# Optimization experiments

Hardware: AMD Instinct MI355X
Metric: run time of the kernel (lower is better)

Reference implementation:

```python
import jax, jax.numpy as jnp
import numpy as np


def setup_inputs() -> dict:
    key = jax.random.key(0)
    ks = jax.random.split(key, 6)
    B, Q, K = 4, 512, 1024
    Dq, Dk, Dv, H = 512, 512, 512, 128
    return {
        "queries": jax.random.normal(ks[0], (B, Q, Dq), dtype=jnp.float32),
        "keys": jax.random.normal(ks[1], (B, K, Dk), dtype=jnp.float32),
        "values": jax.random.normal(ks[2], (B, K, Dv), dtype=jnp.float32),
        "W_q": jax.random.normal(ks[3], (Dq, H), dtype=jnp.float32) / np.sqrt(Dq),
        "W_k": jax.random.normal(ks[4], (Dk, H), dtype=jnp.float32) / np.sqrt(Dk),
        "w_v": jax.random.normal(ks[5], (H,), dtype=jnp.float32) / np.sqrt(H),
    }


def reference(queries, keys, values, W_q, W_k, w_v):
    # Additive (Bahdanau) attention.
    q = jnp.einsum("bqd,dh->bqh", queries, W_q)          # [B,Q,H]
    k = jnp.einsum("bkd,dh->bkh", keys, W_k)             # [B,K,H]
    features = jnp.tanh(q[:, :, None, :] + k[:, None, :, :])  # [B,Q,K,H]
    scores = jnp.einsum("bqkh,h->bqk", features, w_v)    # [B,Q,K]
    attn = jax.nn.softmax(scores, axis=-1)               # [B,Q,K]
    return jnp.einsum("bqk,bkv->bqv", attn, values)      # [B,Q,Dv]
```

## Files before the change

kernel.cpp:

```cpp
#include <hip/hip_runtime.h>

#define BB   4
#define QS   512
#define KSZ  1024
#define DD   512
#define HH   128
#define DVV  512

typedef unsigned int uint;
typedef unsigned short ushort;
typedef __attribute__((ext_vector_type(8)))  short short8;
typedef __attribute__((ext_vector_type(16))) float f32x16;

__device__ __forceinline__ float rcp_fast(float x)  { return __builtin_amdgcn_rcpf(x); }
__device__ __forceinline__ float exp2_fast(float x) { return __builtin_amdgcn_exp2f(x); }

__device__ __forceinline__ void split1(float v, ushort& h, ushort& l) {
    uint u = __float_as_uint(v);
    h = (ushort)(u >> 16);
    float r = v - __uint_as_float(u & 0xffff0000u);
    l = (ushort)(__float_as_uint(r) >> 16);
}

#define NVT (BB * (KSZ / 32) * (DVV / 32))
#define NQ8 (BB * QS / 8)
#define NK8 (BB * KSZ / 8)

__global__ __launch_bounds__(256) void prep_kernel(
    const float* __restrict__ q,  const float* __restrict__ k,
    const float* __restrict__ val,
    const float* __restrict__ Wq, const float* __restrict__ Wk,
    float* __restrict__ eq, float* __restrict__ ek,
    ushort* __restrict__ vhi, ushort* __restrict__ vlo)
{
    const int id  = blockIdx.x;
    const int tid = threadIdx.x;

    if (id < NVT) {
        __shared__ float Ts[32][33];
        const int b   = id >> 9;
        const int rem = id & 511;
        const int k0  = (rem >> 4) * 32;
        const int n0  = (rem & 15) * 32;
        {
            const int kk = tid >> 3, n4 = (tid & 7) * 4;
            float4 v = *(const float4*)&val[((size_t)b * KSZ + k0 + kk) * DVV + n0 + n4];
            Ts[kk][n4 + 0] = v.x; Ts[kk][n4 + 1] = v.y;
            Ts[kk][n4 + 2] = v.z; Ts[kk][n4 + 3] = v.w;
        }
        __syncthreads();
        {
            const int nn = tid >> 3, k4 = (tid & 7) * 4;
            ushort h[4], l[4];
            #pragma unroll
            for (int i = 0; i < 4; i++) split1(Ts[k4 + i][nn], h[i], l[i]);
            size_t o = ((size_t)b * DVV + n0 + nn) * KSZ + k0 + k4;
            *(ushort4*)&vhi[o] = make_ushort4(h[0], h[1], h[2], h[3]);
            *(ushort4*)&vlo[o] = make_ushort4(l[0], l[1], l[2], l[3]);
        }
        return;
    }

    __shared__ float At[8][36];
    __shared__ float Wt[32][128];

    const int pid = id - NVT;
    const float* A; const float* W; float* outp; int m0;
    if (pid < NQ8) { A = q; W = Wq; outp = eq; m0 = pid * 8; }
    else           { A = k; W = Wk; outp = ek; m0 = (pid - NQ8) * 8; }

    const int h4 = tid & 31;
    const int r  = tid >> 5;

    float4 acc = {0.f, 0.f, 0.f, 0.f};

    for (int d0 = 0; d0 < DD; d0 += 32) {
        if (tid < 64) {
            int row = tid >> 3, c4 = tid & 7;
            *(float4*)&At[row][c4 * 4] =
                *(const float4*)&A[(size_t)(m0 + row) * DD + d0 + c4 * 4];
        }
        #pragma unroll
        for (int i = 0; i < 4; i++) {
            int f = tid + i * 256;
            int row = f >> 5, c4 = f & 31;
            *(float4*)&Wt[row][c4 * 4] =
                *(const float4*)&W[(size_t)(d0 + row) * HH + c4 * 4];
        }
        __syncthreads();
        #pragma unroll 8
        for (int kk = 0; kk < 32; kk++) {
            float4 w4 = *(const float4*)&Wt[kk][h4 * 4];
            float a0 = At[r][kk];
            acc.x = fmaf(a0, w4.x, acc.x); acc.y = fmaf(a0, w4.y, acc.y);
            acc.z = fmaf(a0, w4.z, acc.z); acc.w = fmaf(a0, w4.w, acc.w);
        }
        __syncthreads();
    }

    const float C2L = 2.8853900817779268f;
    float4 o;
    o.x = exp2_fast(acc.x * C2L); o.y = exp2_fast(acc.y * C2L);
    o.z = exp2_fast(acc.z * C2L); o.w = exp2_fast(acc.w * C2L);
    *(float4*)&outp[(size_t)(m0 + r) * HH + h4 * 4] = o;
}

__global__ __launch_bounds__(256) void scores_kernel(
    const float* __restrict__ eq, const float* __restrict__ ek,
    const float* __restrict__ wv, ushort* __restrict__ Phi,
    ushort* __restrict__ Plo, float* __restrict__ rsp)
{
    __shared__ float eqs[64][68];
    __shared__ float eks[64][68];

    const int tid = threadIdx.x;
    const int b  = blockIdx.z;
    const int q0 = blockIdx.y * 64;
    const int k0 = blockIdx.x * 64;

    const float* eqb = eq + ((size_t)b * QS  + q0) * HH;
    const float* ekb = ek + ((size_t)b * KSZ + k0) * HH;

    const int tk = tid & 15;
    const int tq = tid >> 4;

    float acc[4][4] = {};

    for (int hc = 0; hc < HH; hc += 64) {
        __syncthreads();
        #pragma unroll
        for (int i = 0; i < 4; i++) {
            int f = tid + i * 256;
            int row = f >> 4, c4 = f & 15;
            *(float4*)&eqs[row][c4 * 4] =
                *(const float4*)&eqb[(size_t)row * HH + hc + c4 * 4];
            *(float4*)&eks[row][c4 * 4] =
                *(const float4*)&ekb[(size_t)row * HH + hc + c4 * 4];
        }
        __syncthreads();

        for (int h0 = 0; h0 < 64; h0 += 4) {
            float4 wv4 = *(const float4*)&wv[hc + h0];
            float4 eq4[4], ek4[4];
            #pragma unroll
            for (int j = 0; j < 4; j++) {
                eq4[j] = *(const float4*)&eqs[tq + 16 * j][h0];
                ek4[j] = *(const float4*)&eks[tk + 16 * j][h0];
            }
            #pragma unroll
            for (int jq = 0; jq < 4; jq++) {
                #pragma unroll
                for (int jk = 0; jk < 4; jk++) {
                    acc[jq][jk] = fmaf(wv4.x, rcp_fast(fmaf(eq4[jq].x, ek4[jk].x, 1.0f)), acc[jq][jk]);
                    acc[jq][jk] = fmaf(wv4.y, rcp_fast(fmaf(eq4[jq].y, ek4[jk].y, 1.0f)), acc[jq][jk]);
                    acc[jq][jk] = fmaf(wv4.z, rcp_fast(fmaf(eq4[jq].z, ek4[jk].z, 1.0f)), acc[jq][jk]);
                    acc[jq][jk] = fmaf(wv4.w, rcp_fast(fmaf(eq4[jq].w, ek4[jk].w, 1.0f)), acc[jq][jk]);
                }
            }
        }
    }

    const float CN = -2.8853900817779268f;
    ushort* ph = Phi + ((size_t)b * QS + q0) * KSZ + k0;
    ushort* pl = Plo + ((size_t)b * QS + q0) * KSZ + k0;
    #pragma unroll
    for (int jq = 0; jq < 4; jq++) {
        float rowp = 0.f;
        #pragma unroll
        for (int jk = 0; jk < 4; jk++) {
            float pv_ = exp2_fast(acc[jq][jk] * CN);
            ushort hh, ll; split1(pv_, hh, ll);
            size_t o = (size_t)(tq + 16 * jq) * KSZ + tk + 16 * jk;
            ph[o] = hh; pl[o] = ll;
            rowp += pv_;
        }
        #pragma unroll
        for (int m = 8; m; m >>= 1) rowp += __shfl_xor(rowp, m);
        if ((tid & 15) == 0)
            rsp[((size_t)b * QS + q0 + tq + 16 * jq) * 16 + blockIdx.x] = rowp;
    }
}

__global__ __launch_bounds__(256) void pv_mfma_kernel(
    const ushort* __restrict__ Phi, const ushort* __restrict__ Plo,
    const ushort* __restrict__ vhi, const ushort* __restrict__ vlo,
    const float* __restrict__ rsp, float* __restrict__ outp)
{
    __shared__ float invs[64];
    __shared__ float accs[2][32][33];

    const int id = blockIdx.x;
    const int x  = id & 7;
    const int j  = id >> 3;
    const int b  = x >> 1;
    const int mt = (x & 1) * 4 + (j >> 4);
    const int nt = j & 15;

    const int tid = threadIdx.x, w = tid >> 6, lane = tid & 63;

    if (tid < 64) {
        const float* rp = rsp + ((size_t)b * QS + mt * 64 + tid) * 16;
        float s = 0.f;
        #pragma unroll
        for (int i = 0; i < 16; i++) s += rp[i];
        invs[tid] = rcp_fast(s);
    }

    const int mw  = mt * 64 + (w & 1) * 32;
    const int kh  = (w >> 1) * (KSZ / 2);
    const int row = lane & 31, kg = lane >> 5;
    const int nb  = nt * 32;

    const ushort* pah = Phi + ((size_t)b * QS  + mw + row) * KSZ + kh;
    const ushort* pal = Plo + ((size_t)b * QS  + mw + row) * KSZ + kh;
    const ushort* bhp = vhi + ((size_t)b * DVV + nb + row) * KSZ + kh;
    const ushort* blp = vlo + ((size_t)b * DVV + nb + row) * KSZ + kh;

    f32x16 acc;
    #pragma unroll
    for (int i = 0; i < 16; i++) acc[i] = 0.f;

    #pragma unroll 8
    for (int kb = 0; kb < KSZ / 2; kb += 16) {
        const int ka = kb + kg * 8;
        short8 ah = *(const short8*)(pah + ka);
        short8 al = *(const short8*)(pal + ka);
        short8 vh = *(const short8*)(bhp + ka);
        short8 vl = *(const short8*)(blp + ka);
        acc = __builtin_amdgcn_mfma_f32_32x32x16_bf16(ah, vh, acc, 0, 0, 0);
        acc = __builtin_amdgcn_mfma_f32_32x32x16_bf16(ah, vl, acc, 0, 0, 0);
        acc = __builtin_amdgcn_mfma_f32_32x32x16_bf16(al, vh, acc, 0, 0, 0);
    }

    if (w >= 2) {
        #pragma unroll
        for (int r = 0; r < 16; r++)
            accs[w - 2][(r & 3) + 8 * (r >> 2) + 4 * kg][row] = acc[r];
    }
    __syncthreads();
    if (w < 2) {
        float* ob = outp + ((size_t)b * QS + mw) * DVV + nb;
        #pragma unroll
        for (int r = 0; r < 16; r++) {
            const int rb = (r & 3) + 8 * (r >> 2) + 4 * kg;
            float v = acc[r] + accs[w][rb][row];
            ob[(size_t)rb * DVV + row] = v * invs[(w & 1) * 32 + rb];
        }
    }
}

extern "C" void kernel_launch(void* const* d_in, const int* in_sizes, int n_in,
                              void* d_out, int out_size, void* d_ws, size_t ws_size,
                              hipStream_t stream)
{
    const float* queries = (const float*)d_in[0];
    const float* keys    = (const float*)d_in[1];
    const float* values  = (const float*)d_in[2];
    const float* Wq      = (const float*)d_in[3];
    const float* Wk      = (const float*)d_in[4];
    const float* wv      = (const float*)d_in[5];
    float* out = (float*)d_out;

    float*  eq  = (float*)d_ws;
    float*  ek  = eq + (size_t)BB * QS * HH;
    float*  rsp = ek + (size_t)BB * KSZ * HH;
    ushort* Phi = (ushort*)(rsp + (size_t)BB * QS * 16);
    ushort* Plo = Phi + (size_t)BB * QS * KSZ;
    ushort* vhi = Plo + (size_t)BB * QS * KSZ;
    ushort* vlo = vhi + (size_t)BB * KSZ * DVV;

    prep_kernel<<<dim3(NVT + NQ8 + NK8), 256, 0, stream>>>(
        queries, keys, values, Wq, Wk, eq, ek, vhi, vlo);

    scores_kernel<<<dim3(KSZ / 64, QS / 64, BB), 256, 0, stream>>>(
        eq, ek, wv, Phi, Plo, rsp);

    pv_mfma_kernel<<<dim3(512), 256, 0, stream>>>(Phi, Plo, vhi, vlo, rsp, out);
}
```

Before: 170.1 us.

## Enlarge projection row tiles and split PV MFMA over four K-quarters

The projection part of prep_kernel now computes 32 rows per block instead of 8, with four accumulators per thread. This reuses each loaded W tile across more rows and cuts the block count. The PV kernel switches from 64x32 output tiles with a 2-way K split to 32x32 tiles with a 4-way K split across waves, launched as 1024 blocks, with explicit software prefetch of the next operands. The partial sums are reduced through shared memory. This trades extra LDS reduction work and more redundant Phi reads for higher parallelism and better latency hiding.

```diff
diff --git a/kernel.cpp b/kernel.cpp
--- a/kernel.cpp
+++ b/kernel.cpp
@@ -22,9 +22,9 @@
     l = (ushort)(__float_as_uint(r) >> 16);
 }
 
-#define NVT (BB * (KSZ / 32) * (DVV / 32))
-#define NQ8 (BB * QS / 8)
-#define NK8 (BB * KSZ / 8)
+#define NVT  (BB * (KSZ / 32) * (DVV / 32))
+#define NQ32 (BB * QS / 32)
+#define NK32 (BB * KSZ / 32)
 
 __global__ __launch_bounds__(256) void prep_kernel(
     const float* __restrict__ q,  const float* __restrict__ k,
@@ -61,21 +61,21 @@
         return;
     }
 
-    __shared__ float At[8][36];
+    __shared__ float At[32][36];
     __shared__ float Wt[32][128];
 
     const int pid = id - NVT;
     const float* A; const float* W; float* outp; int m0;
-    if (pid < NQ8) { A = q; W = Wq; outp = eq; m0 = pid * 8; }
-    else           { A = k; W = Wk; outp = ek; m0 = (pid - NQ8) * 8; }
+    if (pid < NQ32) { A = q; W = Wq; outp = eq; m0 = pid * 32; }
+    else            { A = k; W = Wk; outp = ek; m0 = (pid - NQ32) * 32; }
 
     const int h4 = tid & 31;
     const int r  = tid >> 5;
 
-    float4 acc = {0.f, 0.f, 0.f, 0.f};
+    float4 acc[4] = {};
 
     for (int d0 = 0; d0 < DD; d0 += 32) {
-        if (tid < 64) {
+        {
             int row = tid >> 3, c4 = tid & 7;
             *(float4*)&At[row][c4 * 4] =
                 *(const float4*)&A[(size_t)(m0 + row) * DD + d0 + c4 * 4];
@@ -91,18 +91,26 @@
         #pragma unroll 8
         for (int kk = 0; kk < 32; kk++) {
             float4 w4 = *(const float4*)&Wt[kk][h4 * 4];
-            float a0 = At[r][kk];
-            acc.x = fmaf(a0, w4.x, acc.x); acc.y = fmaf(a0, w4.y, acc.y);
-            acc.z = fmaf(a0, w4.z, acc.z); acc.w = fmaf(a0, w4.w, acc.w);
+            #pragma unroll
+            for (int i = 0; i < 4; i++) {
+                float a = At[r + 8 * i][kk];
+                acc[i].x = fmaf(a, w4.x, acc[i].x);
+                acc[i].y = fmaf(a, w4.y, acc[i].y);
+                acc[i].z = fmaf(a, w4.z, acc[i].z);
+                acc[i].w = fmaf(a, w4.w, acc[i].w);
+            }
         }
         __syncthreads();
     }
 
     const float C2L = 2.8853900817779268f;
-    float4 o;
-    o.x = exp2_fast(acc.x * C2L); o.y = exp2_fast(acc.y * C2L);
-    o.z = exp2_fast(acc.z * C2L); o.w = exp2_fast(acc.w * C2L);
-    *(float4*)&outp[(size_t)(m0 + r) * HH + h4 * 4] = o;
+    #pragma unroll
+    for (int i = 0; i < 4; i++) {
+        float4 o;
+        o.x = exp2_fast(acc[i].x * C2L); o.y = exp2_fast(acc[i].y * C2L);
+        o.z = exp2_fast(acc[i].z * C2L); o.w = exp2_fast(acc[i].w * C2L);
+        *(float4*)&outp[(size_t)(m0 + r + 8 * i) * HH + h4 * 4] = o;
+    }
 }
 
 __global__ __launch_bounds__(256) void scores_kernel(
@@ -186,65 +194,70 @@
     const ushort* __restrict__ vhi, const ushort* __restrict__ vlo,
     const float* __restrict__ rsp, float* __restrict__ outp)
 {
-    __shared__ float invs[64];
-    __shared__ float accs[2][32][33];
+    __shared__ float invs[32];
+    __shared__ float accs[3][32][33];
 
     const int id = blockIdx.x;
     const int x  = id & 7;
     const int j  = id >> 3;
-    const int b  = x >> 1;
-    const int mt = (x & 1) * 4 + (j >> 4);
     const int nt = j & 15;
+    const int bm = x * 8 + (j >> 4);
+    const int b  = bm >> 4, mt = bm & 15;
 
     const int tid = threadIdx.x, w = tid >> 6, lane = tid & 63;
-
-    if (tid < 64) {
-        const float* rp = rsp + ((size_t)b * QS + mt * 64 + tid) * 16;
+    const int row = lane & 31, kg = lane >> 5;
+
+    if (tid < 32) {
+        const float* rp = rsp + ((size_t)b * QS + mt * 32 + tid) * 16;
         float s = 0.f;
         #pragma unroll
         for (int i = 0; i < 16; i++) s += rp[i];
         invs[tid] = rcp_fast(s);
     }
 
-    const int mw  = mt * 64 + (w & 1) * 32;
-    const int kh  = (w >> 1) * (KSZ / 2);
-    const int row = lane & 31, kg = lane >> 5;
-    const int nb  = nt * 32;
-
-    const ushort* pah = Phi + ((size_t)b * QS  + mw + row) * KSZ + kh;
-    const ushort* pal = Plo + ((size_t)b * QS  + mw + row) * KSZ + kh;
-    const ushort* bhp = vhi + ((size_t)b * DVV + nb + row) * KSZ + kh;
-    const ushort* blp = vlo + ((size_t)b * DVV + nb + row) * KSZ + kh;
+    const int kq = w * (KSZ / 4);
+    const ushort* pah = Phi + ((size_t)b * QS  + mt * 32 + row) * KSZ + kq + kg * 8;
+    const ushort* pal = Plo + ((size_t)b * QS  + mt * 32 + row) * KSZ + kq + kg * 8;
+    const ushort* bhp = vhi + ((size_t)b * DVV + nt * 32 + row) * KSZ + kq + kg * 8;
+    const ushort* blp = vlo + ((size_t)b * DVV + nt * 32 + row) * KSZ + kq + kg * 8;
 
     f32x16 acc;
     #pragma unroll
     for (int i = 0; i < 16; i++) acc[i] = 0.f;
 
-    #pragma unroll 8
-    for (int kb = 0; kb < KSZ / 2; kb += 16) {
-        const int ka = kb + kg * 8;
-        short8 ah = *(const short8*)(pah + ka);
-        short8 al = *(const short8*)(pal + ka);
-        short8 vh = *(const short8*)(bhp + ka);
-        short8 vl = *(const short8*)(blp + ka);
+    short8 ah = *(const short8*)pah;
+    short8 al = *(const short8*)pal;
+    short8 vh = *(const short8*)bhp;
+    short8 vl = *(const short8*)blp;
+
+    #pragma unroll
+    for (int it = 1; it < 16; it++) {
+        short8 nah = *(const short8*)(pah + it * 16);
+        short8 nal = *(const short8*)(pal + it * 16);
+        short8 nvh = *(const short8*)(bhp + it * 16);
+        short8 nvl = *(const short8*)(blp + it * 16);
         acc = __builtin_amdgcn_mfma_f32_32x32x16_bf16(ah, vh, acc, 0, 0, 0);
         acc = __builtin_amdgcn_mfma_f32_32x32x16_bf16(ah, vl, acc, 0, 0, 0);
         acc = __builtin_amdgcn_mfma_f32_32x32x16_bf16(al, vh, acc, 0, 0, 0);
-    }
-
-    if (w >= 2) {
+        ah = nah; al = nal; vh = nvh; vl = nvl;
+    }
+    acc = __builtin_amdgcn_mfma_f32_32x32x16_bf16(ah, vh, acc, 0, 0, 0);
+    acc = __builtin_amdgcn_mfma_f32_32x32x16_bf16(ah, vl, acc, 0, 0, 0);
+    acc = __builtin_amdgcn_mfma_f32_32x32x16_bf16(al, vh, acc, 0, 0, 0);
+
+    if (w > 0) {
         #pragma unroll
         for (int r = 0; r < 16; r++)
-            accs[w - 2][(r & 3) + 8 * (r >> 2) + 4 * kg][row] = acc[r];
+            accs[w - 1][(r & 3) + 8 * (r >> 2) + 4 * kg][row] = acc[r];
     }
     __syncthreads();
-    if (w < 2) {
-        float* ob = outp + ((size_t)b * QS + mw) * DVV + nb;
+    if (w == 0) {
+        float* ob = outp + ((size_t)b * QS + mt * 32) * DVV + nt * 32;
         #pragma unroll
         for (int r = 0; r < 16; r++) {
             const int rb = (r & 3) + 8 * (r >> 2) + 4 * kg;
-            float v = acc[r] + accs[w][rb][row];
-            ob[(size_t)rb * DVV + row] = v * invs[(w & 1) * 32 + rb];
+            float v = acc[r] + accs[0][rb][row] + accs[1][rb][row] + accs[2][rb][row];
+            ob[(size_t)rb * DVV + row] = v * invs[rb];
         }
     }
 }
@@ -269,11 +282,11 @@
     ushort* vhi = Plo + (size_t)BB * QS * KSZ;
     ushort* vlo = vhi + (size_t)BB * KSZ * DVV;
 
-    prep_kernel<<<dim3(NVT + NQ8 + NK8), 256, 0, stream>>>(
+    prep_kernel<<<dim3(NVT + NQ32 + NK32), 256, 0, stream>>>(
         queries, keys, values, Wq, Wk, eq, ek, vhi, vlo);
 
     scores_kernel<<<dim3(KSZ / 64, QS / 64, BB), 256, 0, stream>>>(
         eq, ek, wv, Phi, Plo, rsp);
 
-    pv_mfma_kernel<<<dim3(512), 256, 0, stream>>>(Phi, Plo, vhi, vlo, rsp, out);
-}
+    pv_mfma_kernel<<<dim3(1024), 256, 0, stream>>>(Phi, Plo, vhi, vlo, rsp, out);
+}
```

Result: slower. 184.4 us (+8.4%).
